# Optimization experiments

Measured on AMD Instinct MI355X. Metric: run time of the kernel, lower is better.

## Reference

```python
import jax, jax.numpy as jnp
import numpy as np

NT, NS, NH, NG = 365, 1024, 64, 32
NW = NH * 8 + 2


def setup_inputs() -> dict:
    key = jax.random.key(0)
    k1, k2, k3, k4 = jax.random.split(key, 4)
    std = 1.0 / np.sqrt(NH)
    x = jax.random.normal(k1, (NT, NS, 4), dtype=jnp.float32)
    # make P (precip) nonnegative and T1 < T2 plausible-ish; math is still generic
    xc = jax.random.normal(k2, (NS, NG), dtype=jnp.float32)
    fc_w = jax.random.uniform(k3, (NW, NG), minval=-std, maxval=std, dtype=jnp.float32)
    fc_b = jax.random.uniform(k4, (NW,), minval=-std, maxval=std, dtype=jnp.float32)
    return {"x": x, "xc": xc, "fc_w": fc_w, "fc_b": fc_b}


def reference(x, xc, fc_w, fc_b):
    nh = NH
    P, E, T1, T2 = x[..., 0], x[..., 1], x[..., 2], x[..., 3]  # each [nt, ns]
    Ta = (T1 + T2) * 0.5
    # rain/snow partition: rP = 1 - arccos((T1+T2)/(T2-T1))/3.1415, masked
    valid = (T1 < 0) & (T2 > 0)
    denom = jnp.where(valid, T2 - T1, 1.0)
    ratio = jnp.clip(jnp.where(valid, (T1 + T2) / denom, 0.0), -0.999999, 0.999999)
    rP = 1.0 - jnp.arccos(ratio) / 3.1415
    rP = jnp.where(T1 >= 0, 1.0, rP)
    rP = jnp.where(T2 <= 0, 0.0, rP)
    Ps = (1.0 - rP) * P  # snow   [nt, ns]
    Pl = rP * P          # liquid [nt, ns]

    w = xc @ fc_w.T + fc_b  # [ns, nh*8+2]
    gm = jnp.exp(w[:, :nh]) + 1.0
    ge = jax.nn.sigmoid(w[:, nh:2 * nh]) * 2.0
    go = jax.nn.sigmoid(w[:, 2 * nh:3 * nh])
    gl = jnp.exp(w[:, 3 * nh:4 * nh] * 2.0)
    ga = jax.nn.softmax(w[:, 4 * nh:5 * nh], axis=1)  # Dropout in eval mode = identity
    gb = jax.nn.sigmoid(w[:, 5 * nh:6 * nh])
    qb = jax.nn.relu(w[:, -1]) / nh  # [ns]
    kb = jax.nn.sigmoid(w[:, 6 * nh:7 * nh]) / 10.0
    gi = jax.nn.sigmoid(w[:, 7 * nh:8 * nh])

    ns = P.shape[1]
    init = (jnp.zeros((ns, nh), jnp.float32),) * 3  # S0, H0, G0

    def step(carry, inp):
        S0, H0, G0 = carry
        Ps_k, Pl_k, Ta_k, E_k = inp  # each [ns]
        S = S0 + Ps_k[:, None]
        Sm = jnp.minimum(S0, jax.nn.relu(Ta_k[:, None] * gm))  # snowmelt
        H = jax.nn.relu(H0 + Sm + Pl_k[:, None] * gi - E_k[:, None] * ge)
        Q1 = jax.nn.relu(H - gl)
        Q2a = jnp.minimum(H, gl) * go
        Q2 = Q2a * (1.0 - gb)
        G = G0 + Q2a * gb
        Q3 = G * kb
        H0n = jnp.minimum(H - Q2a, gl)
        G0n = G - Q3
        S0n = S - Sm
        Y = jnp.sum((Q1 + Q2 + Q3 + qb[:, None]) * ga, axis=1)  # [ns]
        return (S0n, H0n, G0n), Y

    _, Yout = jax.lax.scan(step, init, (Ps, Pl, Ta, E))
    return Yout  # [nt, ns]
```

## Files before the change

### kernel.cpp

```cpp
#include <hip/hip_runtime.h>
#include <math.h>

#define NT_ 365
#define NS_ 1024
#define NH_ 64
#define NG_ 32
#define NW_ 514
#define CH_ 64
#define NCHUNK_ 6
#define YPAD_ 65

__device__ __forceinline__ float sigmoidf(float v) {
  return 1.0f / (1.0f + expf(-v));
}

__device__ __forceinline__ float rdl(float v, int l) {
  return __int_as_float(__builtin_amdgcn_readlane(__float_as_int(v), l));
}

__device__ __forceinline__ float4 compute_met(float4 xv) {
  const float P = xv.x, E = xv.y, T1 = xv.z, T2 = xv.w;
  const float Ta = (T1 + T2) * 0.5f;
  float rP;
  if (T2 <= 0.0f) {
    rP = 0.0f;
  } else if (T1 >= 0.0f) {
    rP = 1.0f;
  } else {
    float r = (T1 + T2) / (T2 - T1);
    r = fminf(fmaxf(r, -0.999999f), 0.999999f);
    rP = 1.0f - acosf(r) * (1.0f / 3.1415f);
  }
  float4 m;
  m.x = (1.0f - rP) * P;
  m.y = rP * P;
  m.z = fmaxf(Ta, 0.0f);
  m.w = E;
  return m;
}

__global__ __launch_bounds__(256) void waternet_scan(
    const float* __restrict__ x,
    const float* __restrict__ xc,
    const float* __restrict__ fc_w,
    const float* __restrict__ fc_b,
    float* __restrict__ out)
{
  __shared__ float ytile[4][CH_ * YPAD_];

  const int tid  = threadIdx.x;
  const int lane = tid & 63;
  const int wv   = tid >> 6;
  const int site = (blockIdx.x << 2) + wv;
  const int us   = __builtin_amdgcn_readfirstlane(site);
  const float4* xp = (const float4*)x;

  float4 xcur = xp[lane * NS_ + site];

  float acc[8];
#pragma unroll
  for (int k = 0; k < 8; ++k) acc[k] = fc_b[k * NH_ + lane];
  float accq = fc_b[NW_ - 1];

  const float4* xcq = (const float4*)(xc + us * NG_);
  const float4* wq4 = (const float4*)fc_w;
#pragma unroll
  for (int g4 = 0; g4 < NG_ / 4; ++g4) {
    const float4 xv = xcq[g4];
#pragma unroll
    for (int k = 0; k < 8; ++k) {
      const float4 w = wq4[(k * NH_ + lane) * (NG_ / 4) + g4];
      acc[k] = fmaf(xv.x, w.x, acc[k]);
      acc[k] = fmaf(xv.y, w.y, acc[k]);
      acc[k] = fmaf(xv.z, w.z, acc[k]);
      acc[k] = fmaf(xv.w, w.w, acc[k]);
    }
    {
      const float4 w = wq4[(NW_ - 1) * (NG_ / 4) + g4];
      accq = fmaf(xv.x, w.x, accq);
      accq = fmaf(xv.y, w.y, accq);
      accq = fmaf(xv.z, w.z, accq);
      accq = fmaf(xv.w, w.w, accq);
    }
  }

  const float gm  = expf(acc[0]) + 1.0f;
  const float ngm = -gm;
  const float nge = -2.0f * sigmoidf(acc[1]);
  const float go  = sigmoidf(acc[2]);
  const float gl  = expf(acc[3] * 2.0f);
  float mx = acc[4];
#pragma unroll
  for (int m2 = 32; m2 >= 1; m2 >>= 1) mx = fmaxf(mx, __shfl_xor(mx, m2, 64));
  const float ex = expf(acc[4] - mx);
  float sm = ex;
#pragma unroll
  for (int m2 = 32; m2 >= 1; m2 >>= 1) sm += __shfl_xor(sm, m2, 64);
  const float ga = ex / sm;
  const float gb = sigmoidf(acc[5]);
  const float kb = sigmoidf(acc[6]) * 0.1f;
  const float gi = sigmoidf(acc[7]);
  const float qb = fmaxf(accq, 0.0f) * (1.0f / NH_);
  const float mgo  = -go;
  const float kb1m = 1.0f - kb;
  const float cgm  = ga * kb * gb * go;
  const float c1   = ga * (go * (1.0f - gb) - 1.0f);

  float S0 = 0.0f, H0 = 0.0f, Gy = 0.0f;
  float dA, dB;

  float4 mm = compute_met(xcur);

  auto stg = [&](int i, float& dout) {
    const float Ps = rdl(mm.x, i);
    const float Pl = rdl(mm.y, i);
    const float Tz = rdl(mm.z, i);
    const float Ev = rdl(mm.w, i);
    const float a  = fmaf(Tz, ngm, Ps);
    const float Sn = fmaxf(S0 + a, Ps);
    const float Sm = (S0 - Sn) + Ps;
    dout = fmaf(Pl, gi, fmaf(Ev, nge, Sm));
    S0 = Sn;
  };

  auto cns = [&](float d, float* yp) {
    const float z  = H0 + d;
    const float Hh = fmaxf(z, 0.0f);
    const float M  = __builtin_amdgcn_fmed3f(z, 0.0f, gl);
    H0 = fminf(fmaf(mgo, M, Hh), gl);
    Gy = fmaf(kb1m, Gy, cgm * M);
    *yp = Gy + fmaf(c1, M, ga * Hh);
  };

  float*       yw = &ytile[wv][lane];
  const float* yr = &ytile[wv][lane * YPAD_];

  stg(0, dA);

#pragma unroll 1
  for (int c = 0; c < NCHUNK_; ++c) {
    int tn = (c + 1) * CH_ + lane;
    tn = (tn < NT_) ? tn : (NT_ - 1);
    const float4 xnext = xp[tn * NS_ + site];

#pragma unroll
    for (int j2 = 0; j2 < 31; ++j2) {
      const int u = 2 * j2;
      cns(dA, yw + u * YPAD_);
      stg(u + 1, dB);
      cns(dB, yw + (u + 1) * YPAD_);
      stg(u + 2, dA);
    }
    cns(dA, yw + 62 * YPAD_);
    stg(63, dB);
    cns(dB, yw + 63 * YPAD_);

    float r0 = 0.0f, r1 = 0.0f, r2 = 0.0f, r3 = 0.0f;
#pragma unroll
    for (int h = 0; h < CH_; h += 4) {
      r0 += yr[h + 0];
      r1 += yr[h + 1];
      r2 += yr[h + 2];
      r3 += yr[h + 3];
    }
    const int t_out = c * CH_ + lane;
    if (t_out < NT_) out[t_out * NS_ + site] = ((r0 + r1) + (r2 + r3)) + qb;

    if (c + 1 < NCHUNK_) {
      mm = compute_met(xnext);
      stg(0, dA);
    }
  }
}

extern "C" void kernel_launch(void* const* d_in, const int* in_sizes, int n_in,
                              void* d_out, int out_size, void* d_ws, size_t ws_size,
                              hipStream_t stream) {
  const float* x    = (const float*)d_in[0];
  const float* xc   = (const float*)d_in[1];
  const float* fc_w = (const float*)d_in[2];
  const float* fc_b = (const float*)d_in[3];
  float* out = (float*)d_out;

  hipLaunchKernelGGL(waternet_scan, dim3(NS_ / 4), dim3(256), 0, stream,
                     x, xc, fc_w, fc_b, out);
}
```

Baseline: 90.33 us.

## Process two sites per wavefront to interleave independent recurrence chains

Each wavefront now runs the sequential scan for two sites at once, interleaving their dependent chains so one site's latency can be hidden behind the other's instructions. The block shrinks to 128 threads (two waves) while the grid stays the same. This is meant to cut the serial dependency stalls of the scan. In exchange the kernel uses twice as many wavefronts' worth of work per wave, so only half as many waves are live on the GPU (1024 site chains packed into 512 waves), and register pressure goes up.

Measured after the change: 105.6 us. +16.9%, slower.

```diff
diff --git a/kernel.cpp b/kernel.cpp
--- a/kernel.cpp
+++ b/kernel.cpp
@@ -39,7 +39,13 @@
   return m;
 }
 
-__global__ __launch_bounds__(256) void waternet_scan(
+struct Gates {
+  float ngm, nge, gi;
+  float gl, mgo, kb1m, cgm;
+  float ga, c1, qb;
+};
+
+__global__ __launch_bounds__(128) void waternet_scan(
     const float* __restrict__ x,
     const float* __restrict__ xc,
     const float* __restrict__ fc_w,
@@ -51,124 +57,154 @@
   const int tid  = threadIdx.x;
   const int lane = tid & 63;
   const int wv   = tid >> 6;
-  const int site = (blockIdx.x << 2) + wv;
-  const int us   = __builtin_amdgcn_readfirstlane(site);
-  const float4* xp = (const float4*)x;
-
-  float4 xcur = xp[lane * NS_ + site];
-
-  float acc[8];
-#pragma unroll
-  for (int k = 0; k < 8; ++k) acc[k] = fc_b[k * NH_ + lane];
-  float accq = fc_b[NW_ - 1];
-
-  const float4* xcq = (const float4*)(xc + us * NG_);
+  const int ss0  = wv * 2, ss1 = ss0 + 1;
+  const int site0 = (blockIdx.x << 2) + ss0;
+  const int site1 = site0 + 1;
+  const int u0 = __builtin_amdgcn_readfirstlane(site0);
+  const float4* xp  = (const float4*)x;
   const float4* wq4 = (const float4*)fc_w;
+
+  float4 xc0 = xp[lane * NS_ + site0];
+  float4 xc1 = xp[lane * NS_ + site1];
+
+  float a0[8], a1[8];
+#pragma unroll
+  for (int k = 0; k < 8; ++k) { a0[k] = fc_b[k * NH_ + lane]; a1[k] = a0[k]; }
+  float aq0 = fc_b[NW_ - 1], aq1 = aq0;
+
+  const float4* xcq0 = (const float4*)(xc + u0 * NG_);
+  const float4* xcq1 = (const float4*)(xc + (u0 + 1) * NG_);
 #pragma unroll
   for (int g4 = 0; g4 < NG_ / 4; ++g4) {
-    const float4 xv = xcq[g4];
+    const float4 xA = xcq0[g4];
+    const float4 xB = xcq1[g4];
 #pragma unroll
     for (int k = 0; k < 8; ++k) {
       const float4 w = wq4[(k * NH_ + lane) * (NG_ / 4) + g4];
-      acc[k] = fmaf(xv.x, w.x, acc[k]);
-      acc[k] = fmaf(xv.y, w.y, acc[k]);
-      acc[k] = fmaf(xv.z, w.z, acc[k]);
-      acc[k] = fmaf(xv.w, w.w, acc[k]);
+      a0[k] = fmaf(xA.x, w.x, a0[k]); a0[k] = fmaf(xA.y, w.y, a0[k]);
+      a0[k] = fmaf(xA.z, w.z, a0[k]); a0[k] = fmaf(xA.w, w.w, a0[k]);
+      a1[k] = fmaf(xB.x, w.x, a1[k]); a1[k] = fmaf(xB.y, w.y, a1[k]);
+      a1[k] = fmaf(xB.z, w.z, a1[k]); a1[k] = fmaf(xB.w, w.w, a1[k]);
     }
     {
       const float4 w = wq4[(NW_ - 1) * (NG_ / 4) + g4];
-      accq = fmaf(xv.x, w.x, accq);
-      accq = fmaf(xv.y, w.y, accq);
-      accq = fmaf(xv.z, w.z, accq);
-      accq = fmaf(xv.w, w.w, accq);
+      aq0 = fmaf(xA.x, w.x, aq0); aq0 = fmaf(xA.y, w.y, aq0);
+      aq0 = fmaf(xA.z, w.z, aq0); aq0 = fmaf(xA.w, w.w, aq0);
+      aq1 = fmaf(xB.x, w.x, aq1); aq1 = fmaf(xB.y, w.y, aq1);
+      aq1 = fmaf(xB.z, w.z, aq1); aq1 = fmaf(xB.w, w.w, aq1);
     }
   }
 
-  const float gm  = expf(acc[0]) + 1.0f;
-  const float ngm = -gm;
-  const float nge = -2.0f * sigmoidf(acc[1]);
-  const float go  = sigmoidf(acc[2]);
-  const float gl  = expf(acc[3] * 2.0f);
-  float mx = acc[4];
-#pragma unroll
-  for (int m2 = 32; m2 >= 1; m2 >>= 1) mx = fmaxf(mx, __shfl_xor(mx, m2, 64));
-  const float ex = expf(acc[4] - mx);
-  float sm = ex;
-#pragma unroll
-  for (int m2 = 32; m2 >= 1; m2 >>= 1) sm += __shfl_xor(sm, m2, 64);
-  const float ga = ex / sm;
-  const float gb = sigmoidf(acc[5]);
-  const float kb = sigmoidf(acc[6]) * 0.1f;
-  const float gi = sigmoidf(acc[7]);
-  const float qb = fmaxf(accq, 0.0f) * (1.0f / NH_);
-  const float mgo  = -go;
-  const float kb1m = 1.0f - kb;
-  const float cgm  = ga * kb * gb * go;
-  const float c1   = ga * (go * (1.0f - gb) - 1.0f);
-
-  float S0 = 0.0f, H0 = 0.0f, Gy = 0.0f;
-  float dA, dB;
-
-  float4 mm = compute_met(xcur);
-
-  auto stg = [&](int i, float& dout) {
+  auto mkgates = [&](const float a[8], float aq) -> Gates {
+    Gates g;
+    const float gm = expf(a[0]) + 1.0f;
+    g.ngm = -gm;
+    g.nge = -2.0f * sigmoidf(a[1]);
+    const float go = sigmoidf(a[2]);
+    g.gl  = expf(a[3] * 2.0f);
+    float mx = a[4];
+#pragma unroll
+    for (int m2 = 32; m2 >= 1; m2 >>= 1) mx = fmaxf(mx, __shfl_xor(mx, m2, 64));
+    const float ex = expf(a[4] - mx);
+    float sm = ex;
+#pragma unroll
+    for (int m2 = 32; m2 >= 1; m2 >>= 1) sm += __shfl_xor(sm, m2, 64);
+    g.ga = ex / sm;
+    const float gb = sigmoidf(a[5]);
+    const float kb = sigmoidf(a[6]) * 0.1f;
+    g.gi   = sigmoidf(a[7]);
+    g.qb   = fmaxf(aq, 0.0f) * (1.0f / NH_);
+    g.mgo  = -go;
+    g.kb1m = 1.0f - kb;
+    g.cgm  = g.ga * kb * gb * go;
+    g.c1   = g.ga * (go * (1.0f - gb) - 1.0f);
+    return g;
+  };
+  const Gates g0 = mkgates(a0, aq0);
+  const Gates g1 = mkgates(a1, aq1);
+
+  float S0a = 0.f, H0a = 0.f, Gya = 0.f, d0A, d0B;
+  float S0b = 0.f, H0b = 0.f, Gyb = 0.f, d1A, d1B;
+
+  float4 mm0 = compute_met(xc0);
+  float4 mm1 = compute_met(xc1);
+
+  auto stg = [&](const Gates& g, const float4& mm, float& S0, int i,
+                 float& dout) {
     const float Ps = rdl(mm.x, i);
     const float Pl = rdl(mm.y, i);
     const float Tz = rdl(mm.z, i);
     const float Ev = rdl(mm.w, i);
-    const float a  = fmaf(Tz, ngm, Ps);
+    const float a  = fmaf(Tz, g.ngm, Ps);
     const float Sn = fmaxf(S0 + a, Ps);
     const float Sm = (S0 - Sn) + Ps;
-    dout = fmaf(Pl, gi, fmaf(Ev, nge, Sm));
+    dout = fmaf(Pl, g.gi, fmaf(Ev, g.nge, Sm));
     S0 = Sn;
   };
 
-  auto cns = [&](float d, float* yp) {
+  auto cns = [&](const Gates& g, float& H0, float& Gy, float d, float* yp) {
     const float z  = H0 + d;
     const float Hh = fmaxf(z, 0.0f);
-    const float M  = __builtin_amdgcn_fmed3f(z, 0.0f, gl);
-    H0 = fminf(fmaf(mgo, M, Hh), gl);
-    Gy = fmaf(kb1m, Gy, cgm * M);
-    *yp = Gy + fmaf(c1, M, ga * Hh);
+    const float M  = __builtin_amdgcn_fmed3f(z, 0.0f, g.gl);
+    H0 = fminf(fmaf(g.mgo, M, Hh), g.gl);
+    Gy = fmaf(g.kb1m, Gy, g.cgm * M);
+    *yp = Gy + fmaf(g.c1, M, g.ga * Hh);
   };
 
-  float*       yw = &ytile[wv][lane];
-  const float* yr = &ytile[wv][lane * YPAD_];
-
-  stg(0, dA);
+  float*       yw0 = &ytile[ss0][lane];
+  float*       yw1 = &ytile[ss1][lane];
+  const float* yr0 = &ytile[ss0][lane * YPAD_];
+  const float* yr1 = &ytile[ss1][lane * YPAD_];
+
+  stg(g0, mm0, S0a, 0, d0A);
+  stg(g1, mm1, S0b, 0, d1A);
 
 #pragma unroll 1
   for (int c = 0; c < NCHUNK_; ++c) {
     int tn = (c + 1) * CH_ + lane;
     tn = (tn < NT_) ? tn : (NT_ - 1);
-    const float4 xnext = xp[tn * NS_ + site];
+    const float4 xn0 = xp[tn * NS_ + site0];
+    const float4 xn1 = xp[tn * NS_ + site1];
 
 #pragma unroll
     for (int j2 = 0; j2 < 31; ++j2) {
       const int u = 2 * j2;
-      cns(dA, yw + u * YPAD_);
-      stg(u + 1, dB);
-      cns(dB, yw + (u + 1) * YPAD_);
-      stg(u + 2, dA);
-    }
-    cns(dA, yw + 62 * YPAD_);
-    stg(63, dB);
-    cns(dB, yw + 63 * YPAD_);
-
-    float r0 = 0.0f, r1 = 0.0f, r2 = 0.0f, r3 = 0.0f;
+      cns(g0, H0a, Gya, d0A, yw0 + u * YPAD_);
+      cns(g1, H0b, Gyb, d1A, yw1 + u * YPAD_);
+      stg(g0, mm0, S0a, u + 1, d0B);
+      stg(g1, mm1, S0b, u + 1, d1B);
+      cns(g0, H0a, Gya, d0B, yw0 + (u + 1) * YPAD_);
+      cns(g1, H0b, Gyb, d1B, yw1 + (u + 1) * YPAD_);
+      stg(g0, mm0, S0a, u + 2, d0A);
+      stg(g1, mm1, S0b, u + 2, d1A);
+    }
+    cns(g0, H0a, Gya, d0A, yw0 + 62 * YPAD_);
+    cns(g1, H0b, Gyb, d1A, yw1 + 62 * YPAD_);
+    stg(g0, mm0, S0a, 63, d0B);
+    stg(g1, mm1, S0b, 63, d1B);
+    cns(g0, H0a, Gya, d0B, yw0 + 63 * YPAD_);
+    cns(g1, H0b, Gyb, d1B, yw1 + 63 * YPAD_);
+
+    float rA0 = 0.f, rA1 = 0.f, rA2 = 0.f, rA3 = 0.f;
+    float rB0 = 0.f, rB1 = 0.f, rB2 = 0.f, rB3 = 0.f;
 #pragma unroll
     for (int h = 0; h < CH_; h += 4) {
-      r0 += yr[h + 0];
-      r1 += yr[h + 1];
-      r2 += yr[h + 2];
-      r3 += yr[h + 3];
+      rA0 += yr0[h + 0]; rA1 += yr0[h + 1];
+      rA2 += yr0[h + 2]; rA3 += yr0[h + 3];
+      rB0 += yr1[h + 0]; rB1 += yr1[h + 1];
+      rB2 += yr1[h + 2]; rB3 += yr1[h + 3];
     }
     const int t_out = c * CH_ + lane;
-    if (t_out < NT_) out[t_out * NS_ + site] = ((r0 + r1) + (r2 + r3)) + qb;
+    if (t_out < NT_) {
+      out[t_out * NS_ + site0] = ((rA0 + rA1) + (rA2 + rA3)) + g0.qb;
+      out[t_out * NS_ + site1] = ((rB0 + rB1) + (rB2 + rB3)) + g1.qb;
+    }
 
     if (c + 1 < NCHUNK_) {
-      mm = compute_met(xnext);
-      stg(0, dA);
+      mm0 = compute_met(xn0);
+      mm1 = compute_met(xn1);
+      stg(g0, mm0, S0a, 0, d0A);
+      stg(g1, mm1, S0b, 0, d1A);
     }
   }
 }
@@ -182,6 +218,6 @@
   const float* fc_b = (const float*)d_in[3];
   float* out = (float*)d_out;
 
-  hipLaunchKernelGGL(waternet_scan, dim3(NS_ / 4), dim3(256), 0, stream,
+  hipLaunchKernelGGL(waternet_scan, dim3(NS_ / 4), dim3(128), 0, stream,
                      x, xc, fc_w, fc_b, out);
 }
```
